# Kernel tuning notes

Hardware: AMD Instinct MI355X
Metric: run time of the kernel (lower is better)

Reference implementation:

```python
import jax, jax.numpy as jnp
import numpy as np

H = 128; HEADS = 3; OUT = 128
B = 16; N0 = 2048; N1 = 1024; N2 = 512
EPS = 1e-5

def setup_inputs():
    ks = jax.random.split(jax.random.key(0), 16)
    s = 1.0 / np.sqrt(H)
    return {
        "x": jax.random.normal(ks[0], (B * N0, H), jnp.float32),
        "pos": jax.random.normal(ks[1], (B * N0, 3), jnp.float32) * 10.0,
        "bn_gamma": jnp.ones((5, H), jnp.float32),
        "bn_beta": jnp.zeros((5, H), jnp.float32),
        "conv_Wl": jax.random.normal(ks[2], (4, H, HEADS * H), jnp.float32) * s,
        "conv_Wr": jax.random.normal(ks[3], (4, H, HEADS * H), jnp.float32) * s,
        "conv_We": jax.random.normal(ks[4], (4, HEADS * H), jnp.float32) * s,
        "conv_att": jax.random.normal(ks[5], (4, HEADS, H), jnp.float32) * s,
        "conv_bias": jnp.zeros((4, H), jnp.float32),
        "pool_w": jax.random.normal(ks[6], (2, H), jnp.float32) * s,
        "gate_w": jax.random.normal(ks[7], (3, H), jnp.float32) * s,
        "gate_b": jnp.zeros((3,), jnp.float32),
        "ro_w": jax.random.normal(ks[8], (3, H, 2 * H), jnp.float32) * s,
        "ro_b": jnp.zeros((3, 2 * H), jnp.float32),
        "em_w1": jax.random.normal(ks[9], (2, 32), jnp.float32),
        "em_b1": jnp.zeros((2, 32), jnp.float32),
        "em_w2": jax.random.normal(ks[10], (2, 32), jnp.float32) * (1.0 / np.sqrt(32)),
        "em_b2": jnp.zeros((2,), jnp.float32),
        "out_w1": jax.random.normal(ks[11], (6 * H, OUT), jnp.float32) * (1.0 / np.sqrt(6 * H)),
        "out_b1": jnp.zeros((OUT,), jnp.float32),
        "out_w2": jax.random.normal(ks[12], (OUT, OUT), jnp.float32) * (1.0 / np.sqrt(OUT)),
        "out_b2": jnp.zeros((OUT,), jnp.float32),
    }

def _batchnorm(x, g, b):
    mu = x.mean(0)
    var = x.var(0)
    return (x - mu) / jnp.sqrt(var + EPS) * g + b

def _knn_sym_edges(pos, n, k):
    # pos: [B*n, 3], graphs contiguous. knn (loop=True) symmetrized + self loops.
    p = pos.reshape(B, n, 3)
    d2 = jnp.sum((p[:, :, None, :] - p[:, None, :, :]) ** 2, -1)  # [B,n,n]
    _, idx = jax.lax.top_k(-d2, k)  # [B,n,k], self included (dist 0)
    offs = (jnp.arange(B) * n)[:, None, None]
    src = (idx + offs).reshape(-1)  # neighbor (source) nodes
    dst = jnp.broadcast_to(jnp.arange(B * n).reshape(B, n, 1), (B, n, k)).reshape(-1)
    loops = jnp.arange(B * n)
    return jnp.concatenate([src, dst, loops]), jnp.concatenate([dst, src, loops])

def _edge_mlp(pos, src, dst, w1, b1, w2, b2):
    d2 = jnp.sum((pos[src] - pos[dst]) ** 2, -1)
    d = jnp.where(d2 > 0, jnp.sqrt(jnp.where(d2 > 0, d2, 1.0)), 0.0)  # safe norm
    h = jax.nn.relu(d[:, None] * w1[None, :] + b1)  # Linear(1,32)+ReLU
    return jax.nn.relu(h @ w2 + b2)                 # Linear(32,1)+ReLU -> [E]

def _gatv2(h, src, dst, ew, Wl, Wr, We, att, bias):
    N = h.shape[0]
    xl = (h @ Wl).reshape(N, HEADS, H)
    xr = (h @ Wr).reshape(N, HEADS, H)
    z = xl[src] + xr[dst] + ew[:, None, None] * We.reshape(1, HEADS, H)
    z = jax.nn.leaky_relu(z, 0.2)
    logits = jnp.einsum('ehc,hc->eh', z, att)
    m = jax.ops.segment_max(logits, dst, num_segments=N)
    ex = jnp.exp(logits - m[dst])
    denom = jax.ops.segment_sum(ex, dst, num_segments=N)
    alpha = ex / denom[dst]
    out = jax.ops.segment_sum(alpha[:, :, None] * xl[src], dst, num_segments=N)
    return out.mean(1) + bias  # concat=False -> head mean

def _topk_pool(h, w, n, keep):
    score = jax.nn.softmax((h @ w).reshape(B, n), axis=1)  # min_score mode uses softmax per graph
    vals, idx = jax.lax.top_k(score, keep)
    perm = (idx + (jnp.arange(B) * n)[:, None]).reshape(-1)
    return h[perm] * vals.reshape(-1, 1), perm

def _att_agg(h, gw, gb, nw, nb, n):
    alpha = jax.nn.softmax((h @ gw + gb).reshape(B, n), axis=1)
    v = (h @ nw + nb).reshape(B, n, 2 * H)
    return jnp.einsum('bn,bnd->bd', alpha, v)

def _forward(x, pos, bn_gamma, bn_beta, conv_Wl, conv_Wr, conv_We, conv_att, conv_bias, pool_w, gate_w, gate_b, ro_w, ro_b, em_w1, em_b1, em_w2, em_b2, out_w1, out_b1, out_w2, out_b2):
    h = _batchnorm(x, bn_gamma[0], bn_beta[0])
    # stage-0 knn(k=6)+edge_MLP0 is dead in the original forward (pool ignores edges)
    h, perm = _topk_pool(h, pool_w[0], N0, N1)
    pos1 = pos[perm]
    r1 = _att_agg(h, gate_w[0], gate_b[0], ro_w[0], ro_b[0], N1)
    src, dst = _knn_sym_edges(pos1, N1, 10)
    ew = _edge_mlp(pos1, src, dst, em_w1[0], em_b1[0], em_w2[0], em_b2[0])
    h = jax.nn.silu(h + _gatv2(h, src, dst, ew, conv_Wl[0], conv_Wr[0], conv_We[0], conv_att[0], conv_bias[0]))
    h = _batchnorm(h, bn_gamma[1], bn_beta[1])
    h = jax.nn.silu(h + _gatv2(h, src, dst, ew, conv_Wl[1], conv_Wr[1], conv_We[1], conv_att[1], conv_bias[1]))
    h = _batchnorm(h, bn_gamma[2], bn_beta[2])
    h, perm = _topk_pool(h, pool_w[1], N1, N2)
    pos2 = pos1[perm]
    r2 = _att_agg(h, gate_w[1], gate_b[1], ro_w[1], ro_b[1], N2)
    src, dst = _knn_sym_edges(pos2, N2, 10)
    ew = _edge_mlp(pos2, src, dst, em_w1[1], em_b1[1], em_w2[1], em_b2[1])
    h = jax.nn.silu(h + _gatv2(h, src, dst, ew, conv_Wl[2], conv_Wr[2], conv_We[2], conv_att[2], conv_bias[2]))
    h = _batchnorm(h, bn_gamma[3], bn_beta[3])
    h = jax.nn.silu(h + _gatv2(h, src, dst, ew, conv_Wl[3], conv_Wr[3], conv_We[3], conv_att[3], conv_bias[3]))
    h = _batchnorm(h, bn_gamma[4], bn_beta[4])
    r3 = _att_agg(h, gate_w[2], gate_b[2], ro_w[2], ro_b[2], N2)
    cat = jnp.concatenate([r3, r2, r1], axis=1)  # [B, 6H]
    return jax.nn.relu(cat @ out_w1 + out_b1) @ out_w2 + out_b2

def reference(x, pos, bn_gamma, bn_beta, conv_Wl, conv_Wr, conv_We, conv_att, conv_bias, pool_w, gate_w, gate_b, ro_w, ro_b, em_w1, em_b1, em_w2, em_b2, out_w1, out_b1, out_w2, out_b2):
    return _forward(x, pos, bn_gamma, bn_beta, conv_Wl, conv_Wr, conv_We, conv_att, conv_bias, pool_w, gate_w, gate_b, ro_w, ro_b, em_w1, em_b1, em_w2, em_b2, out_w1, out_b1, out_w2, out_b2)
```

## Files before the change

kernel.cpp:

```cpp
#include <hip/hip_runtime.h>
#include <math.h>

#define H 128
#define NHEADS 3
#define BGR 16
#define N0C 2048
#define N1C 1024
#define N2C 512
#define KNN 10
#define EPSV 1e-5f

typedef unsigned short ushortT;
typedef __attribute__((ext_vector_type(8))) short short8;
typedef __attribute__((ext_vector_type(4))) short s16x4;
typedef __attribute__((ext_vector_type(4))) float f32x4;

static __device__ __forceinline__ unsigned short f2bf(float f) {
    unsigned u = __float_as_uint(f);
    unsigned r = (u + 0x7FFF + ((u >> 16) & 1)) >> 16;
    return (unsigned short)r;
}
static __device__ __forceinline__ float bf2f(unsigned short s) {
    return __uint_as_float(((unsigned)s) << 16);
}

static __device__ __forceinline__ int decode_src(int e, int BNK, const int* __restrict__ knn) {
    if (e < BNK) return knn[e];
    int f = e - BNK;
    if (f < BNK) return f / KNN;
    return f - BNK;
}
static __device__ __forceinline__ int decode_dst(int e, int BNK, const int* __restrict__ knn) {
    if (e < BNK) return e / KNN;
    int f = e - BNK;
    if (f < BNK) return knn[f];
    return f - BNK;
}

__global__ void colstats_k(const float* __restrict__ xin, int rows, float* __restrict__ part) {
    int c = threadIdx.x & 127, rr = threadIdx.x >> 7;
    float s = 0.f, q = 0.f;
    for (int r = blockIdx.x * 2 + rr; r < rows; r += 256) {
        float v = xin[(size_t)r * H + c];
        s += v; q += v * v;
    }
    __shared__ float ls[256], lq[256];
    ls[threadIdx.x] = s; lq[threadIdx.x] = q;
    __syncthreads();
    if (rr == 0) {
        part[blockIdx.x * 256 + c]       = s + ls[threadIdx.x + 128];
        part[blockIdx.x * 256 + 128 + c] = q + lq[threadIdx.x + 128];
    }
}
__global__ void colreduce_k(const float* __restrict__ part, float* __restrict__ stats) {
    int t = threadIdx.x;
    float s = 0.f;
    for (int p = 0; p < 128; p++) s += part[p * 256 + t];
    stats[t] = s;
}
__global__ void bn_apply_k(const float* __restrict__ xin, float* __restrict__ xout,
                           ushortT* __restrict__ bfout,
                           const float* __restrict__ stats, const float* __restrict__ g,
                           const float* __restrict__ b, int rows) {
    int idx = blockIdx.x * 256 + threadIdx.x;
    if (idx >= rows * H) return;
    int c = idx & 127;
    float mean = stats[c] / rows;
    float var = stats[128 + c] / rows - mean * mean;
    float v = (xin[idx] - mean) * rsqrtf(var + EPSV) * g[c] + b[c];
    xout[idx] = v;
    if (bfout) bfout[idx] = f2bf(v);
}

__global__ void matvec_k(const float* __restrict__ hsrc, const float* __restrict__ w,
                         const float* __restrict__ bias, float* __restrict__ out, int rows) {
    int wv = blockIdx.x * 4 + (threadIdx.x >> 6);
    int lane = threadIdx.x & 63;
    if (wv >= rows) return;
    float acc = hsrc[(size_t)wv * H + lane] * w[lane] + hsrc[(size_t)wv * H + 64 + lane] * w[64 + lane];
    for (int off = 32; off; off >>= 1) acc += __shfl_xor(acc, off);
    if (lane == 0) out[wv] = acc + (bias ? bias[0] : 0.f);
}

__global__ void pool_softmax_k(const float* __restrict__ logit, int n, float* __restrict__ probs) {
    int b = blockIdx.x, t = threadIdx.x;
    __shared__ float red[256];
    const float* L = logit + b * n;
    float mx = -1e30f;
    for (int i = t; i < n; i += 256) mx = fmaxf(mx, L[i]);
    red[t] = mx; __syncthreads();
    for (int st = 128; st; st >>= 1) { if (t < st) red[t] = fmaxf(red[t], red[t + st]); __syncthreads(); }
    mx = red[0]; __syncthreads();
    float sm = 0.f;
    for (int i = t; i < n; i += 256) sm += expf(L[i] - mx);
    red[t] = sm; __syncthreads();
    for (int st = 128; st; st >>= 1) { if (t < st) red[t] += red[t + st]; __syncthreads(); }
    float inv = 1.f / red[0]; __syncthreads();
    for (int i = t; i < n; i += 256) probs[b * n + i] = expf(L[i] - mx) * inv;
}
__global__ void pool_rank_k(const float* __restrict__ probs, int n, int keep,
                            int* __restrict__ perm, float* __restrict__ vals) {
    __shared__ float s[2048];
    int chunks = n >> 8;
    int b = blockIdx.x / chunks, ch = blockIdx.x % chunks;
    int t = threadIdx.x;
    const float* P = probs + b * n;
    for (int i = t; i < n; i += 256) s[i] = P[i];
    __syncthreads();
    int i = ch * 256 + t;
    float si = s[i];
    int cnt = 0;
    #pragma unroll 4
    for (int j = 0; j < n; j++) {
        float sj = s[j];
        cnt += (sj > si) || (sj == si && j < i);
    }
    if (cnt < keep) { perm[b * keep + cnt] = b * n + i; vals[b * keep + cnt] = si; }
}
__global__ void pool_gather_k(const float* __restrict__ hsrc, const float* __restrict__ possrc,
                              const int* __restrict__ perm, const float* __restrict__ vals,
                              float* __restrict__ hd, ushortT* __restrict__ bfout,
                              float* __restrict__ posd, int rows) {
    int idx = blockIdx.x * 256 + threadIdx.x;
    if (idx >= rows * H) return;
    int r = idx >> 7, c = idx & 127;
    int p = perm[r];
    float v = hsrc[(size_t)p * H + c] * vals[r];
    hd[idx] = v;
    bfout[idx] = f2bf(v);
    if (c < 3) posd[r * 3 + c] = possrc[p * 3 + c];
}

__global__ void att_partial_k(const float* __restrict__ hsrc, const float* __restrict__ probs,
                              int n, float* __restrict__ part) {
    int chunks = n >> 6;
    int b = blockIdx.x / chunks, ch = blockIdx.x % chunks;
    int c = threadIdx.x & 127, rg = threadIdx.x >> 7;
    int r0 = ch * 64;
    float acc = 0.f;
    for (int i = rg; i < 64; i += 2) {
        int r = r0 + i;
        acc += probs[b * n + r] * hsrc[((size_t)b * n + r) * H + c];
    }
    __shared__ float red[256];
    red[threadIdx.x] = acc; __syncthreads();
    if (rg == 0) part[((size_t)b * chunks + ch) * H + c] = red[c] + red[128 + c];
}
__global__ void att_final_k(const float* __restrict__ part, int chunks, float* __restrict__ hbar) {
    int b = blockIdx.x, c = threadIdx.x;
    float s = 0.f;
    for (int ch = 0; ch < chunks; ch++) s += part[((size_t)b * chunks + ch) * H + c];
    hbar[b * H + c] = s;
}
__global__ void ro_gemm_k(const float* __restrict__ hbar, const float* __restrict__ w,
                          const float* __restrict__ bias, float* __restrict__ catp, int coff) {
    int b = blockIdx.x, d = threadIdx.x;
    __shared__ float hb[128];
    if (d < 128) hb[d] = hbar[b * 128 + d];
    __syncthreads();
    float acc = bias[d];
    for (int c = 0; c < 128; c++) acc += hb[c] * w[c * 256 + d];
    catp[b * 768 + coff + d] = acc;
}

__global__ void knn_k(const float* __restrict__ pos, int n, int* __restrict__ knn) {
    int wv = blockIdx.x * 4 + (threadIdx.x >> 6);
    int lane = threadIdx.x & 63;
    int b = wv / n;
    const float* pb = pos + (size_t)b * n * 3;
    float px = pos[(size_t)wv * 3], py = pos[(size_t)wv * 3 + 1], pz = pos[(size_t)wv * 3 + 2];
    int T = n >> 6;
    float d2v[16];
    for (int t = 0; t < T; t++) {
        int j = lane + (t << 6);
        float dx = pb[j * 3] - px, dy = pb[j * 3 + 1] - py, dz = pb[j * 3 + 2] - pz;
        d2v[t] = dx * dx + dy * dy + dz * dz;
    }
    for (int r = 0; r < KNN; r++) {
        float bv = 1e30f; int bt = 0;
        for (int t = 0; t < T; t++)
            if (d2v[t] < bv) { bv = d2v[t]; bt = t; }
        int bidx = lane + (bt << 6);
        for (int off = 32; off; off >>= 1) {
            float ov = __shfl_xor(bv, off);
            int oi = __shfl_xor(bidx, off);
            if (ov < bv || (ov == bv && oi < bidx)) { bv = ov; bidx = oi; }
        }
        if ((bidx & 63) == lane) d2v[bidx >> 6] = 1e30f;
        if (lane == 0) knn[(size_t)wv * KNN + r] = b * n + bidx;
    }
}

__global__ void count_rev_k(const int* __restrict__ knn, int NBK, int* __restrict__ deg) {
    int f = blockIdx.x * 256 + threadIdx.x;
    if (f < NBK) atomicAdd(&deg[knn[f]], 1);
}
__global__ __launch_bounds__(1024) void scan_k(const int* __restrict__ deg, int* __restrict__ off,
                                               int* __restrict__ cur, int NB) {
    __shared__ int part[1024];
    int t = threadIdx.x;
    int per = NB >> 10;
    int base = t * per;
    int s = 0;
    for (int i = 0; i < per; i++) s += deg[base + i] + KNN + 1;
    part[t] = s; __syncthreads();
    for (int d = 1; d < 1024; d <<= 1) {
        int v = (t >= d) ? part[t - d] : 0;
        __syncthreads();
        part[t] += v;
        __syncthreads();
    }
    int prefix = (t > 0) ? part[t - 1] : 0;
    for (int i = 0; i < per; i++) {
        off[base + i] = prefix; cur[base + i] = prefix; prefix += deg[base + i] + KNN + 1;
    }
    if (t == 1023) off[NB] = part[1023];
}
__global__ void fill_eids_k(const int* __restrict__ knn, int NB, int E,
                            int* __restrict__ cur, int* __restrict__ eids,
                            int* __restrict__ dsts) {
    int e = blockIdx.x * 256 + threadIdx.x;
    if (e >= E) return;
    int dst = decode_dst(e, NB * KNN, knn);
    int p = atomicAdd(&cur[dst], 1);
    eids[p] = e;
    dsts[p] = dst;
}
__global__ void rank_gather_k(const int* __restrict__ eids, const int* __restrict__ dsts,
                              const int* __restrict__ off, const int* __restrict__ knn,
                              const float* __restrict__ pos, int NB, int E,
                              const float* __restrict__ w1, const float* __restrict__ b1,
                              const float* __restrict__ w2, const float* __restrict__ b2,
                              int* __restrict__ srcs, float* __restrict__ ews) {
    int o = blockIdx.x * 256 + threadIdx.x;
    if (o >= E) return;
    int e = eids[o];
    int d = dsts[o];
    int o0 = off[d], o1 = off[d + 1];
    int rank = 0;
    for (int q = o0; q < o1; q++) rank += (eids[q] < e);
    int src = decode_src(e, NB * KNN, knn);
    float dx = pos[src * 3] - pos[d * 3];
    float dy = pos[src * 3 + 1] - pos[d * 3 + 1];
    float dz = pos[src * 3 + 2] - pos[d * 3 + 2];
    float d2 = dx * dx + dy * dy + dz * dz;
    float dd = d2 > 0.f ? sqrtf(d2) : 0.f;
    float acc = b2[0];
    #pragma unroll
    for (int k = 0; k < 32; k++) {
        float hh = fmaxf(dd * w1[k] + b1[k], 0.f);
        acc += hh * w2[k];
    }
    srcs[o0 + rank] = src;
    ews[o0 + rank] = fmaxf(acc, 0.f);
}

__global__ void wcvt_all_k(const float* __restrict__ Wl, const float* __restrict__ Wr,
                           ushortT* __restrict__ BT) {
    int i = blockIdx.x * 256 + threadIdx.x;
    if (i >= 4 * 128 * 768) return;
    int layer = i / 98304, rem = i % 98304;
    int k = rem / 768, n = rem % 768;
    const float* W = (n < 384) ? (Wl + (size_t)layer * 128 * 384) : (Wr + (size_t)layer * 128 * 384);
    int nn = (n < 384) ? n : n - 384;
    BT[(size_t)layer * 98304 + (size_t)n * 128 + k] = f2bf(W[k * 384 + nn]);
}

__global__ __launch_bounds__(256) void gemm_mfma_k(const ushortT* __restrict__ A,
                                                   const ushortT* __restrict__ BT,
                                                   ushortT* __restrict__ C, int M) {
    __shared__ ushortT As[128 * 128];
    __shared__ ushortT Bs[128 * 128];
    int nb = blockIdx.x % 6, mb = blockIdx.x / 6;
    int row0 = mb * 128, col0 = nb * 128;
    int tid = threadIdx.x;
    #pragma unroll
    for (int it = 0; it < 8; it++) {
        int idx = tid + it * 256;
        int row = idx >> 4, seg = idx & 15;
        int byte = (row * 256 + seg * 16) ^ ((row & 7) << 4);
        *(float4*)((char*)As + byte) =
            *(const float4*)((const char*)(A + (size_t)(row0 + row) * 128) + seg * 16);
        *(float4*)((char*)Bs + byte) =
            *(const float4*)((const char*)(BT + (size_t)(col0 + row) * 128) + seg * 16);
    }
    __syncthreads();
    int wave = tid >> 6, lane = tid & 63;
    int wr = wave >> 1, wc = wave & 1;
    f32x4 acc[4][4] = {};
    int lrow = lane & 15;
    int lkb = (lane >> 4) * 16;
    #pragma unroll
    for (int ks = 0; ks < 4; ks++) {
        short8 af[4], bfr[4];
        #pragma unroll
        for (int m = 0; m < 4; m++) {
            int row = wr * 64 + m * 16 + lrow;
            int byte = (row * 256 + ks * 64 + lkb) ^ ((row & 7) << 4);
            af[m] = *(short8*)((char*)As + byte);
        }
        #pragma unroll
        for (int n = 0; n < 4; n++) {
            int col = wc * 64 + n * 16 + lrow;
            int byte = (col * 256 + ks * 64 + lkb) ^ ((col & 7) << 4);
            bfr[n] = *(short8*)((char*)Bs + byte);
        }
        #pragma unroll
        for (int m = 0; m < 4; m++)
            #pragma unroll
            for (int n = 0; n < 4; n++)
                acc[m][n] = __builtin_amdgcn_mfma_f32_16x16x32_bf16(af[m], bfr[n], acc[m][n], 0, 0, 0);
    }
    #pragma unroll
    for (int m = 0; m < 4; m++)
        #pragma unroll
        for (int n = 0; n < 4; n++) {
            int r0 = row0 + wr * 64 + m * 16 + (lane >> 4) * 4;
            int c = col0 + wc * 64 + n * 16 + (lane & 15);
            #pragma unroll
            for (int j = 0; j < 4; j++)
                C[(size_t)(r0 + j) * 768 + c] = f2bf(acc[m][n][j]);
        }
}

__global__ void gat_fused_k(const float* __restrict__ hin, const ushortT* __restrict__ xlr,
                            const int* __restrict__ off, const int* __restrict__ srcs,
                            const float* __restrict__ ews, int NB, int n,
                            const float* __restrict__ We, const float* __restrict__ att,
                            const float* __restrict__ bias, float* __restrict__ hout) {
    int bpg = n >> 2;
    int xcd = blockIdx.x & 7, slot = blockIdx.x >> 3;
    int gid = xcd + 8 * (slot / bpg);
    int node = gid * n + (slot % bpg) * 4 + (threadIdx.x >> 6);
    if (node >= NB) return;
    int lane = threadIdx.x & 63;
    int l = lane & 31, half = lane >> 5;
    float wek[3][4], attk[3][4], xrk[3][4];
    const ushortT* xrp = xlr + (size_t)node * 768 + 384;
    #pragma unroll
    for (int j = 0; j < 3; j++) {
        float4 wv = *(const float4*)(We + j * 128 + l * 4);
        float4 av = *(const float4*)(att + j * 128 + l * 4);
        s16x4 xv4 = *(const s16x4*)(xrp + j * 128 + l * 4);
        wek[j][0] = wv.x; wek[j][1] = wv.y; wek[j][2] = wv.z; wek[j][3] = wv.w;
        attk[j][0] = av.x; attk[j][1] = av.y; attk[j][2] = av.z; attk[j][3] = av.w;
        #pragma unroll
        for (int q = 0; q < 4; q++) xrk[j][q] = bf2f((unsigned short)xv4[q]);
    }
    float d[3] = {0.f, 0.f, 0.f};
    float acc[3][4] = {};
    int o0 = off[node], o1 = off[node + 1];
    for (int o = o0 + half; o < o1; o += 2) {
        int src = srcs[o];
        float w = ews[o];
        const ushortT* pl = xlr + (size_t)src * 768;
        float p[3];
        float xv[3][4];
        #pragma unroll
        for (int j = 0; j < 3; j++) {
            s16x4 v = *(const s16x4*)(pl + j * 128 + l * 4);
            float pj = 0.f;
            #pragma unroll
            for (int q = 0; q < 4; q++) {
                float xlv = bf2f((unsigned short)v[q]);
                xv[j][q] = xlv;
                float z = xlv + xrk[j][q] + w * wek[j][q];
                z = z >= 0.f ? z : 0.2f * z;
                pj += z * attk[j][q];
            }
            p[j] = pj;
        }
        #pragma unroll
        for (int sh = 16; sh; sh >>= 1) {
            p[0] += __shfl_xor(p[0], sh);
            p[1] += __shfl_xor(p[1], sh);
            p[2] += __shfl_xor(p[2], sh);
        }
        #pragma unroll
        for (int j = 0; j < 3; j++) {
            float e = __expf(fminf(p[j], 60.f));
            d[j] += e;
            #pragma unroll
            for (int q = 0; q < 4; q++) acc[j][q] += e * xv[j][q];
        }
    }
    #pragma unroll
    for (int j = 0; j < 3; j++) {
        d[j] += __shfl_xor(d[j], 32);
        #pragma unroll
        for (int q = 0; q < 4; q++) acc[j][q] += __shfl_xor(acc[j][q], 32);
    }
    if (half == 0) {
        float4 bv = *(const float4*)(bias + l * 4);
        float4 hv = *(const float4*)(hin + (size_t)node * H + l * 4);
        float i0 = 1.f / d[0], i1 = 1.f / d[1], i2 = 1.f / d[2];
        float bb[4] = {bv.x, bv.y, bv.z, bv.w};
        float hh[4] = {hv.x, hv.y, hv.z, hv.w};
        float ob[4];
        #pragma unroll
        for (int q = 0; q < 4; q++) {
            float g = (acc[0][q] * i0 + acc[1][q] * i1 + acc[2][q] * i2) * (1.f / 3.f) + bb[q];
            float xa = hh[q] + g;
            ob[q] = xa / (1.f + __expf(-xa));
        }
        *(float4*)(hout + (size_t)node * H + l * 4) = make_float4(ob[0], ob[1], ob[2], ob[3]);
    }
}

__global__ void head_k(const float* __restrict__ cat, const float* __restrict__ W1,
                       const float* __restrict__ b1, const float* __restrict__ W2,
                       const float* __restrict__ b2, float* __restrict__ outp) {
    int b = blockIdx.x, d = threadIdx.x;
    __shared__ float cs[768];
    __shared__ float o1[128];
    for (int i = d; i < 768; i += 128) cs[i] = cat[b * 768 + i];
    __syncthreads();
    float s = b1[d];
    for (int c = 0; c < 768; c++) s += cs[c] * W1[c * 128 + d];
    o1[d] = fmaxf(s, 0.f);
    __syncthreads();
    float s2 = b2[d];
    for (int c = 0; c < 128; c++) s2 += o1[c] * W2[c * 128 + d];
    outp[b * 128 + d] = s2;
}

extern "C" void kernel_launch(void* const* d_in, const int* in_sizes, int n_in,
                              void* d_out, int out_size, void* d_ws, size_t ws_size,
                              hipStream_t stream) {
    (void)in_sizes; (void)n_in; (void)out_size; (void)ws_size;
    const float* x        = (const float*)d_in[0];
    const float* pos      = (const float*)d_in[1];
    const float* bn_g     = (const float*)d_in[2];
    const float* bn_b     = (const float*)d_in[3];
    const float* conv_Wl  = (const float*)d_in[4];
    const float* conv_Wr  = (const float*)d_in[5];
    const float* conv_We  = (const float*)d_in[6];
    const float* conv_att = (const float*)d_in[7];
    const float* conv_bias= (const float*)d_in[8];
    const float* pool_w   = (const float*)d_in[9];
    const float* gate_w   = (const float*)d_in[10];
    const float* gate_b   = (const float*)d_in[11];
    const float* ro_w     = (const float*)d_in[12];
    const float* ro_b     = (const float*)d_in[13];
    const float* em_w1    = (const float*)d_in[14];
    const float* em_b1    = (const float*)d_in[15];
    const float* em_w2    = (const float*)d_in[16];
    const float* em_b2    = (const float*)d_in[17];
    const float* out_w1   = (const float*)d_in[18];
    const float* out_b1   = (const float*)d_in[19];
    const float* out_w2   = (const float*)d_in[20];
    const float* out_b2   = (const float*)d_in[21];
    float* outp = (float*)d_out;

    const int E1 = BGR * N1C * KNN * 2 + BGR * N1C;
    char* ws = (char*)d_ws;
    size_t o = 0;
    auto take = [&](size_t bytes) -> char* {
        char* p = ws + o;
        o += (bytes + 255) & ~(size_t)255;
        return p;
    };
    ushortT* xlrb = (ushortT*)take((size_t)16384 * 768 * 2);
    ushortT* hbf  = (ushortT*)take((size_t)16384 * 128 * 2);
    ushortT* wbt4 = (ushortT*)take((size_t)4 * 768 * 128 * 2);
    float* h0     = (float*)take((size_t)32768 * 128 * 4);
    float* h1a    = (float*)take((size_t)16384 * 128 * 4);
    float* h1b    = (float*)take((size_t)16384 * 128 * 4);
    float* h2a    = (float*)take((size_t)8192 * 128 * 4);
    float* h2b    = (float*)take((size_t)8192 * 128 * 4);
    float* ews    = (float*)take((size_t)E1 * 4);
    float* pos1   = (float*)take((size_t)16384 * 3 * 4);
    float* pos2   = (float*)take((size_t)8192 * 3 * 4);
    float* plog   = (float*)take((size_t)32768 * 4);
    float* probs  = (float*)take((size_t)32768 * 4);
    float* vals   = (float*)take((size_t)16384 * 4);
    float* hbar   = (float*)take((size_t)2048 * 4);
    float* apart  = (float*)take((size_t)16 * 32 * 128 * 4);
    float* catb   = (float*)take((size_t)12288 * 4);
    float* stats  = (float*)take((size_t)256 * 4);
    float* parts  = (float*)take((size_t)128 * 256 * 4);
    int* knnb     = (int*)take((size_t)163840 * 4);
    int* permb    = (int*)take((size_t)16384 * 4);
    int* degb     = (int*)take((size_t)16385 * 4);
    int* offb     = (int*)take((size_t)16385 * 4);
    int* curb     = (int*)take((size_t)16384 * 4);
    int* eidsb    = (int*)take((size_t)E1 * 4);
    int* dstsb    = (int*)take((size_t)E1 * 4);
    int* srcsb    = (int*)take((size_t)E1 * 4);

    auto run_bn = [&](const float* in, float* out2, ushortT* bf, int rows, int layer) {
        colstats_k<<<128, 256, 0, stream>>>(in, rows, parts);
        colreduce_k<<<1, 256, 0, stream>>>(parts, stats);
        bn_apply_k<<<(rows * 128) / 256, 256, 0, stream>>>(in, out2, bf, stats, bn_g + layer * H, bn_b + layer * H, rows);
    };
    auto run_pool = [&](const float* hsrc, const float* possrc, float* hdst, float* posdst,
                        int n, int keep, int p) {
        int rows = BGR * n;
        matvec_k<<<rows / 4, 256, 0, stream>>>(hsrc, pool_w + p * H, nullptr, plog, rows);
        pool_softmax_k<<<BGR, 256, 0, stream>>>(plog, n, probs);
        pool_rank_k<<<BGR * (n / 256), 256, 0, stream>>>(probs, n, keep, permb, vals);
        pool_gather_k<<<(BGR * keep * 128) / 256, 256, 0, stream>>>(hsrc, possrc, permb, vals, hdst, hbf, posdst, BGR * keep);
    };
    auto run_readout = [&](const float* hsrc, int n, int g, int catoff) {
        int rows = BGR * n;
        int chunks = n / 64;
        matvec_k<<<rows / 4, 256, 0, stream>>>(hsrc, gate_w + g * H, gate_b + g, plog, rows);
        pool_softmax_k<<<BGR, 256, 0, stream>>>(plog, n, probs);
        att_partial_k<<<BGR * chunks, 256, 0, stream>>>(hsrc, probs, n, apart);
        att_final_k<<<BGR, 128, 0, stream>>>(apart, chunks, hbar);
        ro_gemm_k<<<BGR, 256, 0, stream>>>(hbar, ro_w + (size_t)g * H * 256, ro_b + g * 256, catb, catoff);
    };
    auto build_graph = [&](const float* posb, int n, int st) {
        int NB = BGR * n, E = NB * KNN * 2 + NB;
        knn_k<<<NB / 4, 256, 0, stream>>>(posb, n, knnb);
        hipMemsetAsync(degb, 0, (size_t)NB * 4, stream);
        count_rev_k<<<(NB * KNN) / 256, 256, 0, stream>>>(knnb, NB * KNN, degb);
        scan_k<<<1, 1024, 0, stream>>>(degb, offb, curb, NB);
        fill_eids_k<<<E / 256, 256, 0, stream>>>(knnb, NB, E, curb, eidsb, dstsb);
        rank_gather_k<<<E / 256, 256, 0, stream>>>(eidsb, dstsb, offb, knnb, posb, NB, E,
                                                   em_w1 + st * 32, em_b1 + st * 32,
                                                   em_w2 + st * 32, em_b2 + st, srcsb, ews);
    };
    auto run_gat = [&](const float* hin, float* hout, int NB, int n, int layer) {
        gemm_mfma_k<<<(NB / 128) * 6, 256, 0, stream>>>(hbf, wbt4 + (size_t)layer * 98304, xlrb, NB);
        gat_fused_k<<<NB / 4, 256, 0, stream>>>(hin, xlrb, offb, srcsb, ews, NB, n,
                                                conv_We + layer * 384, conv_att + layer * 384,
                                                conv_bias + layer * H, hout);
    };

    wcvt_all_k<<<1536, 256, 0, stream>>>(conv_Wl, conv_Wr, wbt4);
    run_bn(x, h0, nullptr, BGR * N0C, 0);
    run_pool(h0, pos, h1a, pos1, N0C, N1C, 0);
    run_readout(h1a, N1C, 0, 512);
    build_graph(pos1, N1C, 0);
    run_gat(h1a, h1b, BGR * N1C, N1C, 0);
    run_bn(h1b, h1a, hbf, BGR * N1C, 1);
    run_gat(h1a, h1b, BGR * N1C, N1C, 1);
    run_bn(h1b, h1a, nullptr, BGR * N1C, 2);
    run_pool(h1a, pos1, h2a, pos2, N1C, N2C, 1);
    run_readout(h2a, N2C, 1, 256);
    build_graph(pos2, N2C, 1);
    run_gat(h2a, h2b, BGR * N2C, N2C, 2);
    run_bn(h2b, h2a, hbf, BGR * N2C, 3);
    run_gat(h2a, h2b, BGR * N2C, N2C, 3);
    run_bn(h2b, h2a, nullptr, BGR * N2C, 4);
    run_readout(h2a, N2C, 2, 0);
    head_k<<<BGR, 128, 0, stream>>>(catb, out_w1, out_b1, out_w2, out_b2, outp);
}
```

Measured before the change: 753.2 us.

## Fuse softmax into pool/readout kernels, fold degree counting into knn

Removes the separate softmax kernels: pool_rank_k now ranks raw logits (softmax is monotone) and computes probabilities only for kept nodes, and att_partial_k recomputes the per-graph softmax in each block. att_final_k is merged into ro_gemm_k, and count_rev_k is folded into knn_k via atomics. The knn distance array is fully unrolled to stay in registers, and leaky-relu becomes fmaxf. This cuts several kernel launches and intermediate buffers, at the cost of redundant per-block softmax reductions and fast-math exp.

```diff
diff --git a/kernel.cpp b/kernel.cpp
--- a/kernel.cpp
+++ b/kernel.cpp
@@ -82,30 +82,24 @@
     if (lane == 0) out[wv] = acc + (bias ? bias[0] : 0.f);
 }
 
-__global__ void pool_softmax_k(const float* __restrict__ logit, int n, float* __restrict__ probs) {
-    int b = blockIdx.x, t = threadIdx.x;
+__global__ void pool_rank_k(const float* __restrict__ logit, int n, int keep,
+                            int* __restrict__ perm, float* __restrict__ vals) {
+    __shared__ float s[2048];
     __shared__ float red[256];
+    int chunks = n >> 8;
+    int b = blockIdx.x / chunks, ch = blockIdx.x % chunks;
+    int t = threadIdx.x;
     const float* L = logit + b * n;
     float mx = -1e30f;
-    for (int i = t; i < n; i += 256) mx = fmaxf(mx, L[i]);
+    for (int i = t; i < n; i += 256) { float v = L[i]; s[i] = v; mx = fmaxf(mx, v); }
     red[t] = mx; __syncthreads();
     for (int st = 128; st; st >>= 1) { if (t < st) red[t] = fmaxf(red[t], red[t + st]); __syncthreads(); }
     mx = red[0]; __syncthreads();
     float sm = 0.f;
-    for (int i = t; i < n; i += 256) sm += expf(L[i] - mx);
+    for (int i = t; i < n; i += 256) sm += __expf(s[i] - mx);
     red[t] = sm; __syncthreads();
     for (int st = 128; st; st >>= 1) { if (t < st) red[t] += red[t + st]; __syncthreads(); }
-    float inv = 1.f / red[0]; __syncthreads();
-    for (int i = t; i < n; i += 256) probs[b * n + i] = expf(L[i] - mx) * inv;
-}
-__global__ void pool_rank_k(const float* __restrict__ probs, int n, int keep,
-                            int* __restrict__ perm, float* __restrict__ vals) {
-    __shared__ float s[2048];
-    int chunks = n >> 8;
-    int b = blockIdx.x / chunks, ch = blockIdx.x % chunks;
-    int t = threadIdx.x;
-    const float* P = probs + b * n;
-    for (int i = t; i < n; i += 256) s[i] = P[i];
+    float inv = 1.f / red[0];
     __syncthreads();
     int i = ch * 256 + t;
     float si = s[i];
@@ -115,7 +109,7 @@
         float sj = s[j];
         cnt += (sj > si) || (sj == si && j < i);
     }
-    if (cnt < keep) { perm[b * keep + cnt] = b * n + i; vals[b * keep + cnt] = si; }
+    if (cnt < keep) { perm[b * keep + cnt] = b * n + i; vals[b * keep + cnt] = __expf(si - mx) * inv; }
 }
 __global__ void pool_gather_k(const float* __restrict__ hsrc, const float* __restrict__ possrc,
                               const int* __restrict__ perm, const float* __restrict__ vals,
@@ -131,39 +125,53 @@
     if (c < 3) posd[r * 3 + c] = possrc[p * 3 + c];
 }
 
-__global__ void att_partial_k(const float* __restrict__ hsrc, const float* __restrict__ probs,
+__global__ void att_partial_k(const float* __restrict__ hsrc, const float* __restrict__ plog,
                               int n, float* __restrict__ part) {
+    __shared__ float s[1024];
+    __shared__ float red[256];
     int chunks = n >> 6;
     int b = blockIdx.x / chunks, ch = blockIdx.x % chunks;
-    int c = threadIdx.x & 127, rg = threadIdx.x >> 7;
+    int t = threadIdx.x;
+    const float* L = plog + b * n;
+    float mx = -1e30f;
+    for (int i = t; i < n; i += 256) { float v = L[i]; s[i] = v; mx = fmaxf(mx, v); }
+    red[t] = mx; __syncthreads();
+    for (int st = 128; st; st >>= 1) { if (t < st) red[t] = fmaxf(red[t], red[t + st]); __syncthreads(); }
+    mx = red[0]; __syncthreads();
+    float sm = 0.f;
+    for (int i = t; i < n; i += 256) sm += __expf(s[i] - mx);
+    red[t] = sm; __syncthreads();
+    for (int st = 128; st; st >>= 1) { if (t < st) red[t] += red[t + st]; __syncthreads(); }
+    float inv = 1.f / red[0];
+    __syncthreads();
+    int c = t & 127, rg = t >> 7;
     int r0 = ch * 64;
     float acc = 0.f;
     for (int i = rg; i < 64; i += 2) {
         int r = r0 + i;
-        acc += probs[b * n + r] * hsrc[((size_t)b * n + r) * H + c];
-    }
-    __shared__ float red[256];
-    red[threadIdx.x] = acc; __syncthreads();
+        acc += __expf(s[r] - mx) * inv * hsrc[((size_t)b * n + r) * H + c];
+    }
+    red[t] = acc; __syncthreads();
     if (rg == 0) part[((size_t)b * chunks + ch) * H + c] = red[c] + red[128 + c];
 }
-__global__ void att_final_k(const float* __restrict__ part, int chunks, float* __restrict__ hbar) {
-    int b = blockIdx.x, c = threadIdx.x;
-    float s = 0.f;
-    for (int ch = 0; ch < chunks; ch++) s += part[((size_t)b * chunks + ch) * H + c];
-    hbar[b * H + c] = s;
-}
-__global__ void ro_gemm_k(const float* __restrict__ hbar, const float* __restrict__ w,
-                          const float* __restrict__ bias, float* __restrict__ catp, int coff) {
+__global__ void ro_gemm_k(const float* __restrict__ part, int chunks,
+                          const float* __restrict__ w, const float* __restrict__ bias,
+                          float* __restrict__ catp, int coff) {
     int b = blockIdx.x, d = threadIdx.x;
     __shared__ float hb[128];
-    if (d < 128) hb[d] = hbar[b * 128 + d];
+    if (d < 128) {
+        float s2 = 0.f;
+        for (int ch = 0; ch < chunks; ch++) s2 += part[((size_t)b * chunks + ch) * H + d];
+        hb[d] = s2;
+    }
     __syncthreads();
     float acc = bias[d];
     for (int c = 0; c < 128; c++) acc += hb[c] * w[c * 256 + d];
     catp[b * 768 + coff + d] = acc;
 }
 
-__global__ void knn_k(const float* __restrict__ pos, int n, int* __restrict__ knn) {
+__global__ void knn_k(const float* __restrict__ pos, int n, int* __restrict__ knn,
+                      int* __restrict__ deg) {
     int wv = blockIdx.x * 4 + (threadIdx.x >> 6);
     int lane = threadIdx.x & 63;
     int b = wv / n;
@@ -171,14 +179,20 @@
     float px = pos[(size_t)wv * 3], py = pos[(size_t)wv * 3 + 1], pz = pos[(size_t)wv * 3 + 2];
     int T = n >> 6;
     float d2v[16];
-    for (int t = 0; t < T; t++) {
-        int j = lane + (t << 6);
-        float dx = pb[j * 3] - px, dy = pb[j * 3 + 1] - py, dz = pb[j * 3 + 2] - pz;
-        d2v[t] = dx * dx + dy * dy + dz * dz;
+    #pragma unroll
+    for (int t = 0; t < 16; t++) {
+        if (t < T) {
+            int j = lane + (t << 6);
+            float dx = pb[j * 3] - px, dy = pb[j * 3 + 1] - py, dz = pb[j * 3 + 2] - pz;
+            d2v[t] = dx * dx + dy * dy + dz * dz;
+        } else {
+            d2v[t] = 1e30f;
+        }
     }
     for (int r = 0; r < KNN; r++) {
-        float bv = 1e30f; int bt = 0;
-        for (int t = 0; t < T; t++)
+        float bv = d2v[0]; int bt = 0;
+        #pragma unroll
+        for (int t = 1; t < 16; t++)
             if (d2v[t] < bv) { bv = d2v[t]; bt = t; }
         int bidx = lane + (bt << 6);
         for (int off = 32; off; off >>= 1) {
@@ -186,15 +200,18 @@
             int oi = __shfl_xor(bidx, off);
             if (ov < bv || (ov == bv && oi < bidx)) { bv = ov; bidx = oi; }
         }
-        if ((bidx & 63) == lane) d2v[bidx >> 6] = 1e30f;
-        if (lane == 0) knn[(size_t)wv * KNN + r] = b * n + bidx;
-    }
-}
-
-__global__ void count_rev_k(const int* __restrict__ knn, int NBK, int* __restrict__ deg) {
-    int f = blockIdx.x * 256 + threadIdx.x;
-    if (f < NBK) atomicAdd(&deg[knn[f]], 1);
-}
+        bool win = (bidx & 63) == lane;
+        int wt = bidx >> 6;
+        #pragma unroll
+        for (int t = 0; t < 16; t++)
+            if (win && t == wt) d2v[t] = 1e30f;
+        if (lane == 0) {
+            knn[(size_t)wv * KNN + r] = b * n + bidx;
+            atomicAdd(&deg[b * n + bidx], 1);
+        }
+    }
+}
+
 __global__ __launch_bounds__(1024) void scan_k(const int* __restrict__ deg, int* __restrict__ off,
                                                int* __restrict__ cur, int NB) {
     __shared__ int part[1024];
@@ -365,7 +382,7 @@
                 float xlv = bf2f((unsigned short)v[q]);
                 xv[j][q] = xlv;
                 float z = xlv + xrk[j][q] + w * wek[j][q];
-                z = z >= 0.f ? z : 0.2f * z;
+                z = fmaxf(z, 0.2f * z);
                 pj += z * attk[j][q];
             }
             p[j] = pj;
@@ -472,9 +489,7 @@
     float* pos1   = (float*)take((size_t)16384 * 3 * 4);
     float* pos2   = (float*)take((size_t)8192 * 3 * 4);
     float* plog   = (float*)take((size_t)32768 * 4);
-    float* probs  = (float*)take((size_t)32768 * 4);
     float* vals   = (float*)take((size_t)16384 * 4);
-    float* hbar   = (float*)take((size_t)2048 * 4);
     float* apart  = (float*)take((size_t)16 * 32 * 128 * 4);
     float* catb   = (float*)take((size_t)12288 * 4);
     float* stats  = (float*)take((size_t)256 * 4);
@@ -497,24 +512,20 @@
                         int n, int keep, int p) {
         int rows = BGR * n;
         matvec_k<<<rows / 4, 256, 0, stream>>>(hsrc, pool_w + p * H, nullptr, plog, rows);
-        pool_softmax_k<<<BGR, 256, 0, stream>>>(plog, n, probs);
-        pool_rank_k<<<BGR * (n / 256), 256, 0, stream>>>(probs, n, keep, permb, vals);
+        pool_rank_k<<<BGR * (n / 256), 256, 0, stream>>>(plog, n, keep, permb, vals);
         pool_gather_k<<<(BGR * keep * 128) / 256, 256, 0, stream>>>(hsrc, possrc, permb, vals, hdst, hbf, posdst, BGR * keep);
     };
     auto run_readout = [&](const float* hsrc, int n, int g, int catoff) {
         int rows = BGR * n;
         int chunks = n / 64;
         matvec_k<<<rows / 4, 256, 0, stream>>>(hsrc, gate_w + g * H, gate_b + g, plog, rows);
-        pool_softmax_k<<<BGR, 256, 0, stream>>>(plog, n, probs);
-        att_partial_k<<<BGR * chunks, 256, 0, stream>>>(hsrc, probs, n, apart);
-        att_final_k<<<BGR, 128, 0, stream>>>(apart, chunks, hbar);
-        ro_gemm_k<<<BGR, 256, 0, stream>>>(hbar, ro_w + (size_t)g * H * 256, ro_b + g * 256, catb, catoff);
+        att_partial_k<<<BGR * chunks, 256, 0, stream>>>(hsrc, plog, n, apart);
+        ro_gemm_k<<<BGR, 256, 0, stream>>>(apart, chunks, ro_w + (size_t)g * H * 256, ro_b + g * 256, catb, catoff);
     };
     auto build_graph = [&](const float* posb, int n, int st) {
         int NB = BGR * n, E = NB * KNN * 2 + NB;
-        knn_k<<<NB / 4, 256, 0, stream>>>(posb, n, knnb);
         hipMemsetAsync(degb, 0, (size_t)NB * 4, stream);
-        count_rev_k<<<(NB * KNN) / 256, 256, 0, stream>>>(knnb, NB * KNN, degb);
+        knn_k<<<NB / 4, 256, 0, stream>>>(posb, n, knnb, degb);
         scan_k<<<1, 1024, 0, stream>>>(degb, offb, curb, NB);
         fill_eids_k<<<E / 256, 256, 0, stream>>>(knnb, NB, E, curb, eidsb, dstsb);
         rank_gather_k<<<E / 256, 256, 0, stream>>>(eidsb, dstsb, offb, knnb, posb, NB, E,
```

After: 702.9 us. -6.7%, faster.
